# Kernel tuning notes

Hardware: AMD Instinct MI355X
Metric: run time of the kernel (lower is better)

## Reference

```python
import jax, jax.numpy as jnp
import numpy as np

N_NODES = 50000
N_EDGES = 800000
D_IN = 64
D_HID = 128  # out_channels * expansion(2)
EPS_MSG = 1e-7
EPS_SOFTMAX = 1e-16
EPS_BN = 1e-5
N_LAYERS = 4


def mish(x):
    return x * jnp.tanh(jax.nn.softplus(x))


def setup_inputs() -> dict:
    key = jax.random.key(0)
    ks = jax.random.split(key, 8)
    x = jax.random.normal(ks[0], (N_NODES, D_IN), dtype=jnp.float32)
    edge_index = jax.random.randint(ks[1], (2, N_EDGES), 0, N_NODES, dtype=jnp.int64)
    # Per-layer GENConv MLP params: Linear(64->128), BN(128), ReLU, Linear(128->64)
    s1 = 1.0 / np.sqrt(D_IN)
    s2 = 1.0 / np.sqrt(D_HID)
    W1 = jax.random.uniform(ks[2], (N_LAYERS, D_IN, D_HID), jnp.float32, -s1, s1)
    b1 = jax.random.uniform(ks[3], (N_LAYERS, D_HID), jnp.float32, -s1, s1)
    gamma = jnp.ones((N_LAYERS, D_HID), jnp.float32)
    beta = jnp.zeros((N_LAYERS, D_HID), jnp.float32)
    W2 = jax.random.uniform(ks[4], (N_LAYERS, D_HID, D_IN), jnp.float32, -s2, s2)
    b2 = jax.random.uniform(ks[5], (N_LAYERS, D_IN), jnp.float32, -s2, s2)
    return {"x": x, "edge_index": edge_index, "W1": W1, "b1": b1,
            "gamma": gamma, "beta": beta, "W2": W2, "b2": b2}


def gen_conv(x, src, dst, W1, b1, gamma, beta, W2, b2):
    n = x.shape[0]
    # message: relu(x_j) + eps  -> [E, D]
    msg = jax.nn.relu(x[src]) + EPS_MSG
    # softmax aggregation (t=1) per destination node, per feature channel
    m = jax.ops.segment_max(msg, dst, num_segments=n)
    e = jnp.exp(msg - m[dst])
    denom = jax.ops.segment_sum(e, dst, num_segments=n)[dst] + EPS_SOFTMAX
    alpha = e / denom
    agg = jax.ops.segment_sum(msg * alpha, dst, num_segments=n)
    # residual with destination features, then 2-layer MLP w/ BatchNorm (train mode)
    h = agg + x
    h = h @ W1 + b1
    mu = jnp.mean(h, axis=0)
    var = jnp.var(h, axis=0)  # biased, as torch BN uses for normalization
    h = (h - mu) * jax.lax.rsqrt(var + EPS_BN) * gamma + beta
    h = jax.nn.relu(h)
    return h @ W2 + b2


def reference(x, edge_index, W1, b1, gamma, beta, W2, b2):
    src, dst = edge_index[0], edge_index[1]
    h = x
    for i in range(N_LAYERS):
        h = gen_conv(h, src, dst, W1[i], b1[i], gamma[i], beta[i], W2[i], b2[i])
        if i < N_LAYERS - 1:
            h = mish(h)
    return h
```

## Files before the change

kernel.cpp:

```cpp
#include <hip/hip_runtime.h>
#include <math.h>

#define N_NODES 50000
#define N_EDGES 800000
#define D_IN 64
#define D_HID 128
#define SCAN_B 256
#define N_SB ((N_NODES + SCAN_B - 1) / SCAN_B)
#define NPB 256
#define NB ((N_NODES + NPB - 1) / NPB)
#define P1_BLOCKS 256
#define EPB (N_EDGES / P1_BLOCKS)
#define CAP 8192
#define XCVT_B (N_NODES * D_IN / 4 / 256)

typedef unsigned short u16;
typedef unsigned int u32;
typedef __attribute__((ext_vector_type(8))) short short8;
typedef __attribute__((ext_vector_type(4))) float f32x4;

union U4S8 { uint4 u; short8 s; };

__device__ __forceinline__ float bf2f(u16 u) {
    u32 x = ((u32)u) << 16;
    float f; __builtin_memcpy(&f, &x, 4); return f;
}
__device__ __forceinline__ u16 f2bf(float f) {
    u32 x; __builtin_memcpy(&x, &f, 4);
    x += 0x7fffu + ((x >> 16) & 1u);
    return (u16)(x >> 16);
}
__device__ __forceinline__ u32 pk2(float a, float b) {
    return (u32)f2bf(a) | ((u32)f2bf(b) << 16);
}
__device__ __forceinline__ u32 relu2(u32 w) {
    u32 b = (w >> 15) & 0x00010001u;
    u32 m01 = b ^ 0x00010001u;
    u32 M = (m01 << 16) - m01;
    return w & M;
}

__global__ __launch_bounds__(256) void bin_pass1_kernel(const int* __restrict__ src,
                                                        const int* __restrict__ dst,
                                                        int* __restrict__ deg,
                                                        int* __restrict__ bcnt,
                                                        u32* __restrict__ ebuf,
                                                        float* __restrict__ bn,
                                                        int* __restrict__ esrc) {
    __shared__ int hist[NB];
    __shared__ int base[NB];
    const int tid = threadIdx.x;
    const int e0 = blockIdx.x * EPB, e1 = e0 + EPB;
    for (int b = tid; b < NB; b += 256) hist[b] = 0;
    if (blockIdx.x == 0) {
        ((float4*)bn)[tid] = make_float4(0.f, 0.f, 0.f, 0.f);
        if (tid < 16) esrc[N_EDGES + tid] = 0;
    }
    __syncthreads();
    for (int i = e0 + tid; i < e1; i += 256) {
        int d = dst[i];
        atomicAdd(&deg[d], 1);
        atomicAdd(&hist[d >> 8], 1);
    }
    __syncthreads();
    for (int b = tid; b < NB; b += 256) {
        base[b] = atomicAdd(&bcnt[b], hist[b]);
        hist[b] = 0;
    }
    __syncthreads();
    for (int i = e0 + tid; i < e1; i += 256) {
        int d = dst[i];
        int b = d >> 8;
        int slot = base[b] + atomicAdd(&hist[b], 1);
        ebuf[(size_t)b * CAP + slot] = ((u32)src[i] << 16) | (u32)d;
    }
}

__global__ __launch_bounds__(SCAN_B) void scan_reduce_kernel(const int* __restrict__ deg,
                                                             int* __restrict__ bsum) {
    __shared__ int s[SCAN_B];
    int i = blockIdx.x * SCAN_B + threadIdx.x;
    int v = (i < N_NODES) ? deg[i] : 0;
    s[threadIdx.x] = v;
    __syncthreads();
    #pragma unroll
    for (int o = SCAN_B / 2; o > 0; o >>= 1) {
        if (threadIdx.x < o) s[threadIdx.x] += s[threadIdx.x + o];
        __syncthreads();
    }
    if (threadIdx.x == 0) bsum[blockIdx.x] = s[0];
}

__global__ __launch_bounds__(SCAN_B) void scan_sums_kernel(const int* __restrict__ bsum,
                                                           int* __restrict__ boff) {
    __shared__ int s[SCAN_B];
    int t = threadIdx.x;
    int v = (t < N_SB) ? bsum[t] : 0;
    s[t] = v;
    __syncthreads();
    #pragma unroll
    for (int o = 1; o < SCAN_B; o <<= 1) {
        int u = (t >= o) ? s[t - o] : 0;
        __syncthreads();
        s[t] += u;
        __syncthreads();
    }
    if (t < N_SB) boff[t] = s[t] - v;
}

__global__ __launch_bounds__(SCAN_B) void scan_write_kernel(const int* __restrict__ deg,
                                                            const int* __restrict__ boff,
                                                            int* __restrict__ off) {
    __shared__ int s[SCAN_B];
    int t = threadIdx.x;
    int i = blockIdx.x * SCAN_B + t;
    int v = (i < N_NODES) ? deg[i] : 0;
    s[t] = v;
    __syncthreads();
    #pragma unroll
    for (int o = 1; o < SCAN_B; o <<= 1) {
        int u = (t >= o) ? s[t - o] : 0;
        __syncthreads();
        s[t] += u;
        __syncthreads();
    }
    int incl = s[t] + boff[blockIdx.x];
    if (i < N_NODES) off[i] = incl - v;
    if (i == N_NODES - 1) off[N_NODES] = incl;
}

__global__ __launch_bounds__(256) void p2xw_kernel(const int* __restrict__ off,
                                                   const int* __restrict__ bcnt,
                                                   const u32* __restrict__ ebuf,
                                                   int* __restrict__ esrc,
                                                   const float* __restrict__ x,
                                                   u16* __restrict__ xb,
                                                   u16* __restrict__ rb,
                                                   const float* __restrict__ W1,
                                                   const float* __restrict__ W2,
                                                   u16* __restrict__ w1f,
                                                   u16* __restrict__ w2f) {
    const int tid = threadIdx.x;
    if (blockIdx.x < NB) {
        __shared__ int soff[NPB];
        __shared__ int cur[NPB];
        const int b = blockIdx.x;
        const int n0 = b * NPB;
        soff[tid] = off[min(n0 + tid, N_NODES)];
        cur[tid] = 0;
        __syncthreads();
        const int cnt = bcnt[b];
        const u32* eb = ebuf + (size_t)b * CAP;
        for (int i = tid; i < cnt; i += 256) {
            u32 p = eb[i];
            int dl = (int)(p & 0xFFFFu) - n0;
            int slot = soff[dl] + atomicAdd(&cur[dl], 1);
            esrc[slot] = (int)(p >> 16);
        }
        return;
    }
    if (blockIdx.x < NB + XCVT_B) {
        int i = (blockIdx.x - NB) * 256 + tid;
        float4 v = ((const float4*)x)[i];
        u32 lo = pk2(v.x, v.y), hi = pk2(v.z, v.w);
        ((uint2*)xb)[i] = make_uint2(lo, hi);
        ((uint2*)rb)[i] = make_uint2(relu2(lo), relu2(hi));
        return;
    }
    const int b = blockIdx.x - NB - XCVT_B;
    const int L = b >> 1;
    if ((b & 1) == 0) {
        const float* W = W1 + (size_t)L * 64 * 128;
        u16* outp = w1f + (size_t)L * 8192;
        for (int idx = tid; idx < 1024; idx += 256) {
            int ln = idx & 63, th = idx >> 6;
            int half = th & 1, t = th >> 1;
            int k0 = half * 32 + (ln >> 4) * 8;
            int n = t * 16 + (ln & 15);
            uint4 o;
            o.x = pk2(W[(k0 + 0) * 128 + n], W[(k0 + 1) * 128 + n]);
            o.y = pk2(W[(k0 + 2) * 128 + n], W[(k0 + 3) * 128 + n]);
            o.z = pk2(W[(k0 + 4) * 128 + n], W[(k0 + 5) * 128 + n]);
            o.w = pk2(W[(k0 + 6) * 128 + n], W[(k0 + 7) * 128 + n]);
            *(uint4*)&outp[(size_t)idx * 8] = o;
        }
    } else {
        const float* W = W2 + (size_t)L * 128 * 64;
        u16* outp = w2f + (size_t)L * 8192;
        for (int idx = tid; idx < 1024; idx += 256) {
            int ln = idx & 63, th = idx >> 6;
            int ks = th & 3, t = th >> 2;
            int k0 = ks * 32 + (ln >> 4) * 8;
            int n = t * 16 + (ln & 15);
            uint4 o;
            o.x = pk2(W[(k0 + 0) * 64 + n], W[(k0 + 1) * 64 + n]);
            o.y = pk2(W[(k0 + 2) * 64 + n], W[(k0 + 3) * 64 + n]);
            o.z = pk2(W[(k0 + 4) * 64 + n], W[(k0 + 5) * 64 + n]);
            o.w = pk2(W[(k0 + 6) * 64 + n], W[(k0 + 7) * 64 + n]);
            *(uint4*)&outp[(size_t)idx * 8] = o;
        }
    }
}

__global__ __launch_bounds__(256) void agg_kernel(const u16* __restrict__ xb,
                                                  const u16* __restrict__ rb,
                                                  const int* __restrict__ off,
                                                  const int* __restrict__ esrc,
                                                  u16* __restrict__ h) {
    const int node = blockIdx.x * 4 + (threadIdx.x >> 6);
    const int ln = threadIdx.x & 63;
    const int jb = __builtin_amdgcn_readfirstlane(off[node]);
    const int je = __builtin_amdgcn_readfirstlane(off[node + 1]);
    const float xown = bf2f(xb[(size_t)node * 64 + ln]);
    float s0 = 0.f, s1 = 0.f, t0 = 0.f, t1 = 0.f;
    int j = jb;
    const int nfull = (je - jb) >> 4;
    for (int it = 0; it < nfull; ++it, j += 16) {
        #pragma unroll
        for (int kk = 0; kk < 16; kk += 2) {
            int i0 = esrc[j + kk];
            int i1 = esrc[j + kk + 1];
            float m0 = bf2f(rb[(size_t)i0 * 64 + ln]);
            float m1 = bf2f(rb[(size_t)i1 * 64 + ln]);
            float p0 = __expf(m0);
            float p1 = __expf(m1);
            s0 += p0; t0 = fmaf(m0, p0, t0);
            s1 += p1; t1 = fmaf(m1, p1, t1);
        }
    }
    const int rem = je - j;
    if (rem > 0) {
        #pragma unroll
        for (int kk = 0; kk < 16; kk += 2) {
            int i0 = esrc[j + kk];
            int i1 = esrc[j + kk + 1];
            float m0 = bf2f(rb[(size_t)i0 * 64 + ln]);
            float m1 = bf2f(rb[(size_t)i1 * 64 + ln]);
            float p0 = (kk < rem)     ? __expf(m0) : 0.f;
            float p1 = (kk + 1 < rem) ? __expf(m1) : 0.f;
            s0 += p0; t0 = fmaf(m0, p0, t0);
            s1 += p1; t1 = fmaf(m1, p1, t1);
        }
    }
    const float s = s0 + s1, t = t0 + t1;
    const float v = t / (s + 1e-16f) + 1e-7f + xown;
    h[(size_t)node * 64 + ln] = f2bf(v);
}

#define SC1 136
__global__ __launch_bounds__(256) void gemm1_kernel(const u16* __restrict__ A,
                                                    const u16* __restrict__ Wf,
                                                    const float* __restrict__ bias,
                                                    u16* __restrict__ Bout,
                                                    float* __restrict__ S,
                                                    float* __restrict__ Q) {
    __shared__ u16 sC[64 * SC1];
    __shared__ float sRed[2][4][128];
    const int tid = threadIdx.x;
    const int wave = tid >> 6, ln = tid & 63;
    const int lm = ln & 15, quad = ln >> 4;
    const int row0g = blockIdx.x * 64;
    const int row0 = row0g + wave * 16;
    const int rA = min(row0 + lm, N_NODES - 1);

    U4S8 a0, a1;
    a0.u = *(const uint4*)&A[(size_t)rA * 64 + quad * 8];
    a1.u = *(const uint4*)&A[(size_t)rA * 64 + 32 + quad * 8];

    f32x4 acc[8];
    #pragma unroll
    for (int t = 0; t < 8; t++) {
        float b = bias[t * 16 + lm];
        acc[t] = (f32x4){b, b, b, b};
    }
    #pragma unroll
    for (int t = 0; t < 8; t++) {
        U4S8 b0, b1;
        b0.u = *(const uint4*)&Wf[(size_t)((t * 2 + 0) * 64 + ln) * 8];
        b1.u = *(const uint4*)&Wf[(size_t)((t * 2 + 1) * 64 + ln) * 8];
        acc[t] = __builtin_amdgcn_mfma_f32_16x16x32_bf16(a0.s, b0.s, acc[t], 0, 0, 0);
        acc[t] = __builtin_amdgcn_mfma_f32_16x16x32_bf16(a1.s, b1.s, acc[t], 0, 0, 0);
    }
    const int rbase = row0 + quad * 4;
    #pragma unroll
    for (int t = 0; t < 8; t++) {
        float ss = 0.f, qq = 0.f;
        #pragma unroll
        for (int rg = 0; rg < 4; rg++) {
            if (rbase + rg < N_NODES) {
                float v = acc[t][rg];
                ss += v; qq = fmaf(v, v, qq);
            }
        }
        ss += __shfl_xor(ss, 16); ss += __shfl_xor(ss, 32);
        qq += __shfl_xor(qq, 16); qq += __shfl_xor(qq, 32);
        if (quad == 0) {
            sRed[0][wave][t * 16 + lm] = ss;
            sRed[1][wave][t * 16 + lm] = qq;
        }
    }
    const int lr0 = wave * 16 + quad * 4;
    #pragma unroll
    for (int t = 0; t < 8; t++) {
        #pragma unroll
        for (int rg = 0; rg < 4; rg++)
            sC[(lr0 + rg) * SC1 + t * 16 + lm] = f2bf(acc[t][rg]);
    }
    __syncthreads();
    const int c8 = (tid & 15) * 8;
    #pragma unroll
    for (int i = 0; i < 4; i++) {
        int lr = (tid >> 4) + i * 16;
        int r = row0g + lr;
        if (r < N_NODES)
            *(uint4*)&Bout[(size_t)r * 128 + c8] = *(const uint4*)&sC[lr * SC1 + c8];
    }
    if (tid < 128) {
        float v = sRed[0][0][tid] + sRed[0][1][tid] + sRed[0][2][tid] + sRed[0][3][tid];
        atomicAdd(&S[tid], v);
    } else {
        int c = tid - 128;
        float v = sRed[1][0][c] + sRed[1][1][c] + sRed[1][2][c] + sRed[1][3][c];
        atomicAdd(&Q[c], v);
    }
}

__device__ __forceinline__ float mish_f(float v) {
    if (v > 30.f) return v;
    float u = __expf(v);
    float t = (u + 1.f) * (u + 1.f);
    return v * (t - 1.f) / (t + 1.f);
}

#define SC2B 72
#define SC2F 68
__global__ __launch_bounds__(256) void gemm2_kernel(const u16* __restrict__ H,
                                                    const float* __restrict__ S,
                                                    const float* __restrict__ Q,
                                                    const float* __restrict__ gamma,
                                                    const float* __restrict__ beta,
                                                    const u16* __restrict__ Wf,
                                                    const float* __restrict__ bias,
                                                    float* __restrict__ outf,
                                                    u16* __restrict__ xb,
                                                    u16* __restrict__ rb,
                                                    int dobf16) {
    __shared__ float sss[256];
    __shared__ __align__(16) char sCraw[64 * SC2F * 4];
    u16* sCb = (u16*)sCraw;
    float* sCf = (float*)sCraw;
    const int tid = threadIdx.x;
    if (tid < 128) {
        float mean = S[tid] * (1.f / N_NODES);
        float var = fmaxf(Q[tid] * (1.f / N_NODES) - mean * mean, 0.f);
        float sc = gamma[tid] * rsqrtf(var + 1e-5f);
        sss[tid] = sc;
        sss[128 + tid] = beta[tid] - mean * sc;
    }
    __syncthreads();
    const int wave = tid >> 6, ln = tid & 63;
    const int lm = ln & 15, quad = ln >> 4;
    const int row0g = blockIdx.x * 64;
    const int row0 = row0g + wave * 16;
    const int rA = min(row0 + lm, N_NODES - 1);

    f32x4 acc[4];
    #pragma unroll
    for (int t = 0; t < 4; t++) {
        float b = bias[t * 16 + lm];
        acc[t] = (f32x4){b, b, b, b};
    }
    #pragma unroll
    for (int ks = 0; ks < 4; ks++) {
        const int k0 = ks * 32 + quad * 8;
        U4S8 h8;
        h8.u = *(const uint4*)&H[(size_t)rA * 128 + k0];
        U4S8 a;
        #pragma unroll
        for (int j2 = 0; j2 < 4; j2++) {
            int k = k0 + 2 * j2;
            float v0 = fmaxf(fmaf(bf2f((u16)h8.s[2 * j2]),     sss[k],     sss[128 + k]),     0.f);
            float v1 = fmaxf(fmaf(bf2f((u16)h8.s[2 * j2 + 1]), sss[k + 1], sss[128 + k + 1]), 0.f);
            ((u32*)&a.u)[j2] = pk2(v0, v1);
        }
        #pragma unroll
        for (int t = 0; t < 4; t++) {
            U4S8 b;
            b.u = *(const uint4*)&Wf[(size_t)((t * 4 + ks) * 64 + ln) * 8];
            acc[t] = __builtin_amdgcn_mfma_f32_16x16x32_bf16(a.s, b.s, acc[t], 0, 0, 0);
        }
    }
    const int lr0 = wave * 16 + quad * 4;
    if (dobf16) {
        #pragma unroll
        for (int t = 0; t < 4; t++) {
            #pragma unroll
            for (int rg = 0; rg < 4; rg++)
                sCb[(lr0 + rg) * SC2B + t * 16 + lm] = f2bf(mish_f(acc[t][rg]));
        }
        __syncthreads();
        const int c8 = (tid & 7) * 8;
        #pragma unroll
        for (int i = 0; i < 2; i++) {
            int lr = (tid >> 3) + i * 32;
            int r = row0g + lr;
            if (r < N_NODES) {
                uint4 val = *(const uint4*)&sCb[lr * SC2B + c8];
                *(uint4*)&xb[(size_t)r * 64 + c8] = val;
                uint4 rv;
                rv.x = relu2(val.x); rv.y = relu2(val.y);
                rv.z = relu2(val.z); rv.w = relu2(val.w);
                *(uint4*)&rb[(size_t)r * 64 + c8] = rv;
            }
        }
    } else {
        #pragma unroll
        for (int t = 0; t < 4; t++) {
            #pragma unroll
            for (int rg = 0; rg < 4; rg++)
                sCf[(lr0 + rg) * SC2F + t * 16 + lm] = acc[t][rg];
        }
        __syncthreads();
        const int c8 = (tid & 7) * 8;
        #pragma unroll
        for (int i = 0; i < 2; i++) {
            int lr = (tid >> 3) + i * 32;
            int r = row0g + lr;
            if (r < N_NODES) {
                *(float4*)&outf[(size_t)r * 64 + c8]     = *(const float4*)&sCf[lr * SC2F + c8];
                *(float4*)&outf[(size_t)r * 64 + c8 + 4] = *(const float4*)&sCf[lr * SC2F + c8 + 4];
            }
        }
    }
}


extern "C" void kernel_launch(void* const* d_in, const int* in_sizes, int n_in,
                              void* d_out, int out_size, void* d_ws, size_t ws_size,
                              hipStream_t stream) {
    const float* x     = (const float*)d_in[0];
    const int*   ei    = (const int*)d_in[1];
    const float* W1    = (const float*)d_in[2];
    const float* b1    = (const float*)d_in[3];
    const float* gamma = (const float*)d_in[4];
    const float* beta  = (const float*)d_in[5];
    const float* W2    = (const float*)d_in[6];
    const float* b2    = (const float*)d_in[7];
    float* out = (float*)d_out;

    const int* src = ei;
    const int* dst = ei + N_EDGES;

    char* base = (char*)d_ws;
    size_t o = 0;
    auto take = [&](size_t bytes) -> char* {
        char* p = base + o;
        o = (o + bytes + 255) & ~(size_t)255;
        return p;
    };
    int* deg     = (int*)take((size_t)(N_NODES + NB) * 4);
    int* bcnt    = deg + N_NODES;
    int* off     = (int*)take((size_t)(N_NODES + 1) * 4);
    int* esrc    = (int*)take((size_t)(N_EDGES + 16) * 4);
    u32* ebuf    = (u32*)take((size_t)NB * CAP * 4);
    int* bsum    = (int*)take((size_t)N_SB * 4);
    int* boff    = (int*)take((size_t)N_SB * 4);
    float* bn    = (float*)take(1024 * 4);
    u16* w1f     = (u16*)take((size_t)4 * 8192 * 2);
    u16* w2f     = (u16*)take((size_t)4 * 8192 * 2);
    u16* xbuf    = (u16*)take((size_t)N_NODES * D_IN * 2);
    u16* rbuf    = (u16*)take((size_t)N_NODES * D_IN * 2);
    u16* hbuf    = (u16*)take((size_t)N_NODES * D_IN * 2);
    u16* h1buf   = (u16*)take((size_t)N_NODES * D_HID * 2);

    hipMemsetAsync(deg, 0, (size_t)(N_NODES + NB) * 4, stream);
    bin_pass1_kernel<<<P1_BLOCKS, 256, 0, stream>>>(src, dst, deg, bcnt, ebuf, bn, esrc);
    scan_reduce_kernel<<<N_SB, SCAN_B, 0, stream>>>(deg, bsum);
    scan_sums_kernel<<<1, SCAN_B, 0, stream>>>(bsum, boff);
    scan_write_kernel<<<N_SB, SCAN_B, 0, stream>>>(deg, boff, off);
    p2xw_kernel<<<NB + XCVT_B + 8, 256, 0, stream>>>(off, bcnt, ebuf, esrc,
                                                     x, xbuf, rbuf,
                                                     W1, W2, w1f, w2f);

    const int NBLK = (N_NODES + 63) / 64;
    const int ABLK = (N_NODES + 3) / 4;
    for (int L = 0; L < 4; L++) {
        float* Sb = bn + L * 256;
        float* Qb = Sb + 128;
        agg_kernel<<<ABLK, 256, 0, stream>>>(xbuf, rbuf, off, esrc, hbuf);
        gemm1_kernel<<<NBLK, 256, 0, stream>>>(
            hbuf, w1f + (size_t)L * 8192, b1 + (size_t)L * D_HID, h1buf,
            Sb, Qb);
        gemm2_kernel<<<NBLK, 256, 0, stream>>>(
            h1buf, Sb, Qb, gamma + (size_t)L * D_HID, beta + (size_t)L * D_HID,
            w2f + (size_t)L * 8192, b2 + (size_t)L * D_IN,
            out, xbuf, rbuf, (L < 3) ? 1 : 0);
    }
}
```

Measured before the change: 386.0 us.

## Fold degree count and prefix scan into bucket pass, drop scan kernels

The global per-node degree atomics and the three scan kernels are removed. Each bucket block in the second pass now computes its global base by reducing the bucket counts of earlier buckets, counts per-node degrees locally from the binned edges in shared memory, and scans them to produce CSR offsets itself. Bucket counters are padded so each sits in its own cache line to reduce atomic contention, and the first pass uses more blocks. This removes three launches and 800k global atomics, at the cost of an extra read of each bucket's edges and redundant base reductions per block.

```diff
diff --git a/kernel.cpp b/kernel.cpp
--- a/kernel.cpp
+++ b/kernel.cpp
@@ -5,13 +5,12 @@
 #define N_EDGES 800000
 #define D_IN 64
 #define D_HID 128
-#define SCAN_B 256
-#define N_SB ((N_NODES + SCAN_B - 1) / SCAN_B)
 #define NPB 256
 #define NB ((N_NODES + NPB - 1) / NPB)
-#define P1_BLOCKS 256
+#define P1_BLOCKS 800
 #define EPB (N_EDGES / P1_BLOCKS)
 #define CAP 8192
+#define BCS 32
 #define XCVT_B (N_NODES * D_IN / 4 / 256)
 
 typedef unsigned short u16;
@@ -42,7 +41,6 @@
 
 __global__ __launch_bounds__(256) void bin_pass1_kernel(const int* __restrict__ src,
                                                         const int* __restrict__ dst,
-                                                        int* __restrict__ deg,
                                                         int* __restrict__ bcnt,
                                                         u32* __restrict__ ebuf,
                                                         float* __restrict__ bn,
@@ -57,14 +55,11 @@
         if (tid < 16) esrc[N_EDGES + tid] = 0;
     }
     __syncthreads();
-    for (int i = e0 + tid; i < e1; i += 256) {
-        int d = dst[i];
-        atomicAdd(&deg[d], 1);
-        atomicAdd(&hist[d >> 8], 1);
-    }
+    for (int i = e0 + tid; i < e1; i += 256)
+        atomicAdd(&hist[dst[i] >> 8], 1);
     __syncthreads();
     for (int b = tid; b < NB; b += 256) {
-        base[b] = atomicAdd(&bcnt[b], hist[b]);
+        base[b] = atomicAdd(&bcnt[b * BCS], hist[b]);
         hist[b] = 0;
     }
     __syncthreads();
@@ -76,60 +71,7 @@
     }
 }
 
-__global__ __launch_bounds__(SCAN_B) void scan_reduce_kernel(const int* __restrict__ deg,
-                                                             int* __restrict__ bsum) {
-    __shared__ int s[SCAN_B];
-    int i = blockIdx.x * SCAN_B + threadIdx.x;
-    int v = (i < N_NODES) ? deg[i] : 0;
-    s[threadIdx.x] = v;
-    __syncthreads();
-    #pragma unroll
-    for (int o = SCAN_B / 2; o > 0; o >>= 1) {
-        if (threadIdx.x < o) s[threadIdx.x] += s[threadIdx.x + o];
-        __syncthreads();
-    }
-    if (threadIdx.x == 0) bsum[blockIdx.x] = s[0];
-}
-
-__global__ __launch_bounds__(SCAN_B) void scan_sums_kernel(const int* __restrict__ bsum,
-                                                           int* __restrict__ boff) {
-    __shared__ int s[SCAN_B];
-    int t = threadIdx.x;
-    int v = (t < N_SB) ? bsum[t] : 0;
-    s[t] = v;
-    __syncthreads();
-    #pragma unroll
-    for (int o = 1; o < SCAN_B; o <<= 1) {
-        int u = (t >= o) ? s[t - o] : 0;
-        __syncthreads();
-        s[t] += u;
-        __syncthreads();
-    }
-    if (t < N_SB) boff[t] = s[t] - v;
-}
-
-__global__ __launch_bounds__(SCAN_B) void scan_write_kernel(const int* __restrict__ deg,
-                                                            const int* __restrict__ boff,
-                                                            int* __restrict__ off) {
-    __shared__ int s[SCAN_B];
-    int t = threadIdx.x;
-    int i = blockIdx.x * SCAN_B + t;
-    int v = (i < N_NODES) ? deg[i] : 0;
-    s[t] = v;
-    __syncthreads();
-    #pragma unroll
-    for (int o = 1; o < SCAN_B; o <<= 1) {
-        int u = (t >= o) ? s[t - o] : 0;
-        __syncthreads();
-        s[t] += u;
-        __syncthreads();
-    }
-    int incl = s[t] + boff[blockIdx.x];
-    if (i < N_NODES) off[i] = incl - v;
-    if (i == N_NODES - 1) off[N_NODES] = incl;
-}
-
-__global__ __launch_bounds__(256) void p2xw_kernel(const int* __restrict__ off,
+__global__ __launch_bounds__(256) void p2xw_kernel(int* __restrict__ off,
                                                    const int* __restrict__ bcnt,
                                                    const u32* __restrict__ ebuf,
                                                    int* __restrict__ esrc,
@@ -142,19 +84,45 @@
                                                    u16* __restrict__ w2f) {
     const int tid = threadIdx.x;
     if (blockIdx.x < NB) {
+        __shared__ int s[NPB];
+        __shared__ int sdeg[NPB];
         __shared__ int soff[NPB];
-        __shared__ int cur[NPB];
         const int b = blockIdx.x;
         const int n0 = b * NPB;
-        soff[tid] = off[min(n0 + tid, N_NODES)];
-        cur[tid] = 0;
-        __syncthreads();
-        const int cnt = bcnt[b];
+        s[tid] = (tid < b) ? bcnt[tid * BCS] : 0;
+        sdeg[tid] = 0;
+        __syncthreads();
+        #pragma unroll
+        for (int o = 128; o > 0; o >>= 1) {
+            if (tid < o) s[tid] += s[tid + o];
+            __syncthreads();
+        }
+        const int sbase = s[0];
+        const int cnt = bcnt[b * BCS];
         const u32* eb = ebuf + (size_t)b * CAP;
+        for (int i = tid; i < cnt; i += 256)
+            atomicAdd(&sdeg[(int)(eb[i] & 0xFFFFu) - n0], 1);
+        __syncthreads();
+        const int v = sdeg[tid];
+        s[tid] = v;
+        __syncthreads();
+        #pragma unroll
+        for (int o = 1; o < NPB; o <<= 1) {
+            int u = (tid >= o) ? s[tid - o] : 0;
+            __syncthreads();
+            s[tid] += u;
+            __syncthreads();
+        }
+        const int go = sbase + s[tid] - v;
+        soff[tid] = go;
+        if (n0 + tid < N_NODES) off[n0 + tid] = go;
+        if (b == 0 && tid == 0) off[N_NODES] = N_EDGES;
+        sdeg[tid] = 0;
+        __syncthreads();
         for (int i = tid; i < cnt; i += 256) {
             u32 p = eb[i];
             int dl = (int)(p & 0xFFFFu) - n0;
-            int slot = soff[dl] + atomicAdd(&cur[dl], 1);
+            int slot = soff[dl] + atomicAdd(&sdeg[dl], 1);
             esrc[slot] = (int)(p >> 16);
         }
         return;
@@ -458,13 +426,10 @@
         o = (o + bytes + 255) & ~(size_t)255;
         return p;
     };
-    int* deg     = (int*)take((size_t)(N_NODES + NB) * 4);
-    int* bcnt    = deg + N_NODES;
+    int* bcnt    = (int*)take((size_t)NB * BCS * 4);
     int* off     = (int*)take((size_t)(N_NODES + 1) * 4);
     int* esrc    = (int*)take((size_t)(N_EDGES + 16) * 4);
     u32* ebuf    = (u32*)take((size_t)NB * CAP * 4);
-    int* bsum    = (int*)take((size_t)N_SB * 4);
-    int* boff    = (int*)take((size_t)N_SB * 4);
     float* bn    = (float*)take(1024 * 4);
     u16* w1f     = (u16*)take((size_t)4 * 8192 * 2);
     u16* w2f     = (u16*)take((size_t)4 * 8192 * 2);
@@ -473,11 +438,8 @@
     u16* hbuf    = (u16*)take((size_t)N_NODES * D_IN * 2);
     u16* h1buf   = (u16*)take((size_t)N_NODES * D_HID * 2);
 
-    hipMemsetAsync(deg, 0, (size_t)(N_NODES + NB) * 4, stream);
-    bin_pass1_kernel<<<P1_BLOCKS, 256, 0, stream>>>(src, dst, deg, bcnt, ebuf, bn, esrc);
-    scan_reduce_kernel<<<N_SB, SCAN_B, 0, stream>>>(deg, bsum);
-    scan_sums_kernel<<<1, SCAN_B, 0, stream>>>(bsum, boff);
-    scan_write_kernel<<<N_SB, SCAN_B, 0, stream>>>(deg, boff, off);
+    hipMemsetAsync(bcnt, 0, (size_t)NB * BCS * 4, stream);
+    bin_pass1_kernel<<<P1_BLOCKS, 256, 0, stream>>>(src, dst, bcnt, ebuf, bn, esrc);
     p2xw_kernel<<<NB + XCVT_B + 8, 256, 0, stream>>>(off, bcnt, ebuf, esrc,
                                                      x, xbuf, rbuf,
                                                      W1, W2, w1f, w2f);
```

Result: faster. 351.1 us (median of 2 runs) (-9.1%).
